# Kernel optimization log

Measured on AMD Instinct MI355X. Metric: run time of the kernel, lower is better.

## Reference

```python
import jax, jax.numpy as jnp
import numpy as np

D_MODEL = 128
REDUCTION = 4
KSIZE = 3
B = D_MODEL  # required by the original code's groups=B conv shape constraint
L = 4096


def setup_inputs() -> dict:
    key = jax.random.key(0)
    ks = jax.random.split(key, 7)
    d, r, K = D_MODEL, REDUCTION, KSIZE
    return {
        "x": jax.random.normal(ks[0], (B, L, d), dtype=jnp.float32),
        "W1": jax.random.normal(ks[1], (d // r, d), dtype=jnp.float32) * (1.0 / np.sqrt(d)),
        "b1": jax.random.normal(ks[2], (d // r,), dtype=jnp.float32) * 0.01,
        "W2": jax.random.normal(ks[3], (K, d // r), dtype=jnp.float32) * (1.0 / np.sqrt(d // r)),
        "b2": jax.random.normal(ks[4], (K,), dtype=jnp.float32) * 0.01,
        "Wc": jax.random.normal(ks[5], (d, d), dtype=jnp.float32) * (1.0 / np.sqrt(d)),
        "bc": jax.random.normal(ks[6], (d,), dtype=jnp.float32) * 0.01,
    }


def reference(x, W1, b1, W2, b2, Wc, bc):
    # x: [B, L, d] with B == d (required by original groups=B conv)
    Bsz, Lseq, d = x.shape
    K = W2.shape[0]
    pad = (K - 1) // 2
    # kernel generation from global average pool
    m = x.mean(axis=1)                                   # [B, d]
    h = jax.nn.gelu(m @ W1.T + b1, approximate=False)    # [B, d//r]
    w = jax.nn.softmax(h @ W2.T + b2, axis=-1)           # [B, K]; row j is the kernel for channel j
    # depthwise-style cross-correlation: y[b, l, c] = sum_k xp[b, l+k, c] * w[c, k]
    xp = jnp.pad(x, ((0, 0), (pad, pad), (0, 0)))        # [B, L+2*pad, d]
    y = sum(xp[:, k:k + Lseq, :] * w[None, None, :, k] for k in range(K))  # [B, L, d]
    # pointwise conv (kernel_size=1) == per-token linear
    return y @ Wc.T + bc                                 # [B, L, d]
```

## Files before the change

### kernel.cpp

```cpp
#include <hip/hip_runtime.h>
#include <hip/hip_bf16.h>

#define D_MODEL 128
#define SEQ_L   4096
#define BATCH   128
#define NSTRIP  2
#define STRIP   (SEQ_L / NSTRIP)
#define NBLK    (BATCH * NSTRIP)

typedef float f4 __attribute__((ext_vector_type(4)));
typedef float f32x4 __attribute__((ext_vector_type(4)));
typedef short bf16x8 __attribute__((ext_vector_type(8)));

__device__ __forceinline__ unsigned short f2bf(float f) {
    union { float f; unsigned u; } v; v.f = f;
    unsigned r = v.u + 0x7FFFu + ((v.u >> 16) & 1u);
    return (unsigned short)(r >> 16);
}

__device__ __forceinline__ void gridbar(int* ctr) {
    __syncthreads();
    if (threadIdx.x == 0) {
        __threadfence();
        atomicAdd(ctr, 1);
        while (__hip_atomic_load(ctr, __ATOMIC_ACQUIRE, __HIP_MEMORY_SCOPE_AGENT) < NBLK)
            __builtin_amdgcn_s_sleep(1);
    }
    __syncthreads();
    __threadfence();
}

template<bool GUARD>
__device__ __forceinline__ void load6(const float* __restrict__ xb, int gr0, int c4, f4 R[6]) {
    #pragma unroll
    for (int j = 0; j < 6; ++j) {
        int gr = gr0 + j;
        if (GUARD) {
            bool ok = (gr >= 0) && (gr < SEQ_L);
            int grc = ok ? gr : 0;
            f4 v = reinterpret_cast<const f4*>(xb + (size_t)grc * D_MODEL)[c4];
            f4 z = {0.f, 0.f, 0.f, 0.f};
            R[j] = ok ? v : z;
        } else {
            R[j] = reinterpret_cast<const f4*>(xb + (size_t)gr * D_MODEL)[c4];
        }
    }
}

__global__ __launch_bounds__(512, 2) void fused(const float* __restrict__ x,
                                                const float* __restrict__ W1,
                                                const float* __restrict__ b1,
                                                const float* __restrict__ W2,
                                                const float* __restrict__ b2,
                                                const float* __restrict__ Wc,
                                                const float* __restrict__ bc,
                                                float* __restrict__ out,
                                                int* __restrict__ ctr,
                                                float* __restrict__ part) {
    __shared__ f4 red[512];
    __shared__ __align__(16) unsigned short y_lds[2][64][132];
    __shared__ __align__(16) float wv_lds[3][128];

    const int t = threadIdx.x, gid = blockIdx.x;
    const int b = gid >> 1, strip = gid & 1;
    const int sb = strip * STRIP;
    const float* xb = x + (size_t)b * SEQ_L * D_MODEL;
    float* outb = out + (size_t)b * SEQ_L * D_MODEL;

    {
        int c4 = t & 31, ph = t >> 5;
        const f4* xv = reinterpret_cast<const f4*>(xb);
        f4 acc = {0.f, 0.f, 0.f, 0.f};
        for (int o = 0; o < STRIP / 128; ++o) {
            f4 R[8];
            #pragma unroll
            for (int j = 0; j < 8; ++j)
                R[j] = xv[(size_t)(sb + o * 128 + ph + j * 16) * 32 + c4];
            R[0] += R[4]; R[1] += R[5]; R[2] += R[6]; R[3] += R[7];
            R[0] += R[2]; R[1] += R[3];
            acc += R[0] + R[1];
        }
        red[t] = acc;
        __syncthreads();
        if (t < 32) {
            f4 s = red[t];
            #pragma unroll
            for (int p = 1; p < 16; ++p) s += red[t + 32 * p];
            reinterpret_cast<f4*>(part + ((size_t)b * NSTRIP + strip) * D_MODEL)[t] = s;
        }
    }
    gridbar(ctr);

    {
        int c = t >> 2, p = t & 3;
        f4 mv[8];
        #pragma unroll
        for (int d4 = 0; d4 < 8; ++d4) mv[d4] = (f4){0.f, 0.f, 0.f, 0.f};
        #pragma unroll
        for (int s = 0; s < NSTRIP; ++s) {
            const f4* ps = reinterpret_cast<const f4*>(part + ((size_t)c * NSTRIP + s) * D_MODEL + p * 32);
            #pragma unroll
            for (int d4 = 0; d4 < 8; ++d4) mv[d4] += ps[d4];
        }
        #pragma unroll
        for (int d4 = 0; d4 < 8; ++d4) mv[d4] *= (1.0f / (float)SEQ_L);

        float h[32];
        #pragma unroll
        for (int j = 0; j < 32; ++j) {
            const f4* w1r = reinterpret_cast<const f4*>(W1 + j * 128 + p * 32);
            f4 s4 = {0.f, 0.f, 0.f, 0.f};
            #pragma unroll
            for (int d4 = 0; d4 < 8; ++d4) s4 += mv[d4] * w1r[d4];
            float s = s4[0] + s4[1] + s4[2] + s4[3];
            s += __shfl_xor(s, 1);
            s += __shfl_xor(s, 2);
            s += b1[j];
            h[j] = 0.5f * s * (1.0f + erff(s * 0.70710678118654752f));
        }
        if (p == 0) {
            float lg[3], mx = -1e30f;
            #pragma unroll
            for (int k = 0; k < 3; ++k) {
                float s = b2[k];
                #pragma unroll
                for (int j = 0; j < 32; ++j) s += h[j] * W2[k * 32 + j];
                lg[k] = s; mx = fmaxf(mx, s);
            }
            float e[3], den = 0.f;
            #pragma unroll
            for (int k = 0; k < 3; ++k) { e[k] = __expf(lg[k] - mx); den += e[k]; }
            float inv = 1.0f / den;
            #pragma unroll
            for (int k = 0; k < 3; ++k) wv_lds[k][c] = e[k] * inv;
        }
    }
    __syncthreads();

    {
        int c4 = t & 31, rg = t >> 5;
        int lane = t & 63, wid = t >> 6;
        int r = lane & 15, q = lane >> 4, kb = q * 8;
        int co0 = wid * 16;

        f4 w0 = *reinterpret_cast<const f4*>(&wv_lds[0][c4 * 4]);
        f4 w1 = *reinterpret_cast<const f4*>(&wv_lds[1][c4 * 4]);
        f4 w2 = *reinterpret_cast<const f4*>(&wv_lds[2][c4 * 4]);

        bf16x8 awc[4];
        #pragma unroll
        for (int kc = 0; kc < 4; ++kc) {
            const float* wr = Wc + (size_t)(co0 + r) * D_MODEL + kc * 32 + kb;
            f4 a = *reinterpret_cast<const f4*>(wr);
            f4 bb = *reinterpret_cast<const f4*>(wr + 4);
            bf16x8 fr;
            fr[0] = (short)f2bf(a[0]); fr[1] = (short)f2bf(a[1]);
            fr[2] = (short)f2bf(a[2]); fr[3] = (short)f2bf(a[3]);
            fr[4] = (short)f2bf(bb[0]); fr[5] = (short)f2bf(bb[1]);
            fr[6] = (short)f2bf(bb[2]); fr[7] = (short)f2bf(bb[3]);
            awc[kc] = fr;
        }

        f4 bcv = *reinterpret_cast<const f4*>(bc + co0 + q * 4);

        f4 R[6];
        if (sb == 0) load6<true>(xb, sb + rg * 4 - 1, c4, R);
        else         load6<false>(xb, sb + rg * 4 - 1, c4, R);

        for (int ht = 0; ht < STRIP / 64; ++ht) {
            const int buf = ht & 1;
            int base = sb + ht * 64;
            #pragma unroll
            for (int j = 0; j < 4; ++j) {
                f4 y = R[j] * w0 + R[j + 1] * w1 + R[j + 2] * w2;
                ushort4 yb;
                yb.x = f2bf(y[0]); yb.y = f2bf(y[1]); yb.z = f2bf(y[2]); yb.w = f2bf(y[3]);
                *reinterpret_cast<ushort4*>(&y_lds[buf][rg * 4 + j][c4 * 4]) = yb;
            }
            if (ht < STRIP / 64 - 1) {
                int nb = base + 64;
                if (nb + 64 == SEQ_L) load6<true>(xb, nb + rg * 4 - 1, c4, R);
                else                  load6<false>(xb, nb + rg * 4 - 1, c4, R);
            }
            __syncthreads();

            f32x4 acc[4];
            #pragma unroll
            for (int g = 0; g < 4; ++g) acc[g] = (f32x4){0.f, 0.f, 0.f, 0.f};
            #pragma unroll
            for (int g = 0; g < 4; ++g)
                #pragma unroll
                for (int kc = 0; kc < 4; ++kc) {
                    bf16x8 bv = *reinterpret_cast<const bf16x8*>(&y_lds[buf][g * 16 + r][kc * 32 + kb]);
                    acc[g] = __builtin_amdgcn_mfma_f32_16x16x32_bf16(awc[kc], bv, acc[g], 0, 0, 0);
                }

            #pragma unroll
            for (int g = 0; g < 4; ++g) {
                int tok = base + g * 16 + r;
                *reinterpret_cast<f4*>(outb + (size_t)tok * D_MODEL + co0 + q * 4) = acc[g] + bcv;
            }
            __syncthreads();
        }
    }
}

extern "C" void kernel_launch(void* const* d_in, const int* in_sizes, int n_in,
                              void* d_out, int out_size, void* d_ws, size_t ws_size,
                              hipStream_t stream) {
    const float* x  = (const float*)d_in[0];
    const float* W1 = (const float*)d_in[1];
    const float* b1 = (const float*)d_in[2];
    const float* W2 = (const float*)d_in[3];
    const float* b2 = (const float*)d_in[4];
    const float* Wc = (const float*)d_in[5];
    const float* bc = (const float*)d_in[6];
    float* out = (float*)d_out;

    char* ws = (char*)d_ws;
    int* ctr = (int*)ws;
    float* part = (float*)(ws + 1024);

    hipMemsetAsync(ctr, 0, 128, stream);
    fused<<<NBLK, 512, 0, stream>>>(x, W1, b1, W2, b2, Wc, bc, out, ctr, part);
}
```

Measured before the change: 271.6 us.

## Split fused grid-barrier kernel into separate mean and conv kernels with finer grids

Replaces the single persistent kernel, which used a software grid barrier across 256 blocks, with two launches. The first computes per-segment channel sums over 8 segments per batch. The second tiles each sequence into 512-token blocks, recomputing the small MLP and softmax per block before the depthwise conv and the MFMA pointwise GEMM. This removes the grid-wide spin barrier and raises the block count to improve latency hiding and load balance. It also double-buffers the register prefetch and drops the second __syncthreads per tile. The cost is redundant MLP and Wc-conversion work in every conv block, plus an extra launch.

```diff
diff --git a/kernel.cpp b/kernel.cpp
--- a/kernel.cpp
+++ b/kernel.cpp
@@ -4,9 +4,8 @@
 #define D_MODEL 128
 #define SEQ_L   4096
 #define BATCH   128
-#define NSTRIP  2
-#define STRIP   (SEQ_L / NSTRIP)
-#define NBLK    (BATCH * NSTRIP)
+#define NSEG    8
+#define TOKS2   512
 
 typedef float f4 __attribute__((ext_vector_type(4)));
 typedef float f32x4 __attribute__((ext_vector_type(4)));
@@ -18,16 +17,33 @@
     return (unsigned short)(r >> 16);
 }
 
-__device__ __forceinline__ void gridbar(int* ctr) {
+__global__ __launch_bounds__(256) void kmean(const float* __restrict__ x,
+                                             float* __restrict__ part) {
+    int seg = blockIdx.x, b = blockIdx.y, t = threadIdx.x;
+    int c4 = t & 31, ph = t >> 5;
+    const f4* xb = reinterpret_cast<const f4*>(x + (size_t)b * SEQ_L * D_MODEL);
+    int l0 = seg * (SEQ_L / NSEG);
+
+    f4 acc = {0.f, 0.f, 0.f, 0.f};
+    #pragma unroll
+    for (int o = 0; o < (SEQ_L / NSEG) / 64; ++o) {
+        f4 R[8];
+        #pragma unroll
+        for (int j = 0; j < 8; ++j)
+            R[j] = xb[(size_t)(l0 + o * 64 + ph + j * 8) * 32 + c4];
+        R[0] += R[4]; R[1] += R[5]; R[2] += R[6]; R[3] += R[7];
+        R[0] += R[2]; R[1] += R[3];
+        acc += R[0] + R[1];
+    }
+    __shared__ f4 red[256];
+    red[t] = acc;
     __syncthreads();
-    if (threadIdx.x == 0) {
-        __threadfence();
-        atomicAdd(ctr, 1);
-        while (__hip_atomic_load(ctr, __ATOMIC_ACQUIRE, __HIP_MEMORY_SCOPE_AGENT) < NBLK)
-            __builtin_amdgcn_s_sleep(1);
-    }
-    __syncthreads();
-    __threadfence();
+    if (t < 32) {
+        f4 s = red[t];
+        #pragma unroll
+        for (int p = 1; p < 8; ++p) s += red[t + 32 * p];
+        reinterpret_cast<f4*>(part + ((size_t)b * NSEG + seg) * D_MODEL)[t] = s;
+    }
 }
 
 template<bool GUARD>
@@ -47,49 +63,31 @@
     }
 }
 
-__global__ __launch_bounds__(512, 2) void fused(const float* __restrict__ x,
+__global__ __launch_bounds__(512, 2) void kconv(const float* __restrict__ x,
+                                                const float* __restrict__ part,
                                                 const float* __restrict__ W1,
                                                 const float* __restrict__ b1,
                                                 const float* __restrict__ W2,
                                                 const float* __restrict__ b2,
                                                 const float* __restrict__ Wc,
                                                 const float* __restrict__ bc,
-                                                float* __restrict__ out,
-                                                int* __restrict__ ctr,
-                                                float* __restrict__ part) {
-    __shared__ f4 red[512];
+                                                float* __restrict__ out) {
     __shared__ __align__(16) unsigned short y_lds[2][64][132];
     __shared__ __align__(16) float wv_lds[3][128];
 
-    const int t = threadIdx.x, gid = blockIdx.x;
-    const int b = gid >> 1, strip = gid & 1;
-    const int sb = strip * STRIP;
+    const int t = threadIdx.x, b = blockIdx.y;
+    const int sb = blockIdx.x * TOKS2;
     const float* xb = x + (size_t)b * SEQ_L * D_MODEL;
     float* outb = out + (size_t)b * SEQ_L * D_MODEL;
 
-    {
-        int c4 = t & 31, ph = t >> 5;
-        const f4* xv = reinterpret_cast<const f4*>(xb);
-        f4 acc = {0.f, 0.f, 0.f, 0.f};
-        for (int o = 0; o < STRIP / 128; ++o) {
-            f4 R[8];
-            #pragma unroll
-            for (int j = 0; j < 8; ++j)
-                R[j] = xv[(size_t)(sb + o * 128 + ph + j * 16) * 32 + c4];
-            R[0] += R[4]; R[1] += R[5]; R[2] += R[6]; R[3] += R[7];
-            R[0] += R[2]; R[1] += R[3];
-            acc += R[0] + R[1];
-        }
-        red[t] = acc;
-        __syncthreads();
-        if (t < 32) {
-            f4 s = red[t];
-            #pragma unroll
-            for (int p = 1; p < 16; ++p) s += red[t + 32 * p];
-            reinterpret_cast<f4*>(part + ((size_t)b * NSTRIP + strip) * D_MODEL)[t] = s;
-        }
-    }
-    gridbar(ctr);
+    int c4 = t & 31, rg = t >> 5;
+    int lane = t & 63, wid = t >> 6;
+    int r = lane & 15, q = lane >> 4, kb = q * 8;
+    int co0 = wid * 16;
+
+    f4 R[2][6];
+    if (sb == 0) load6<true>(xb, sb + rg * 4 - 1, c4, R[0]);
+    else         load6<false>(xb, sb + rg * 4 - 1, c4, R[0]);
 
     {
         int c = t >> 2, p = t & 3;
@@ -97,8 +95,8 @@
         #pragma unroll
         for (int d4 = 0; d4 < 8; ++d4) mv[d4] = (f4){0.f, 0.f, 0.f, 0.f};
         #pragma unroll
-        for (int s = 0; s < NSTRIP; ++s) {
-            const f4* ps = reinterpret_cast<const f4*>(part + ((size_t)c * NSTRIP + s) * D_MODEL + p * 32);
+        for (int s = 0; s < NSEG; ++s) {
+            const f4* ps = reinterpret_cast<const f4*>(part + ((size_t)c * NSEG + s) * D_MODEL + p * 32);
             #pragma unroll
             for (int d4 = 0; d4 < 8; ++d4) mv[d4] += ps[d4];
         }
@@ -137,70 +135,58 @@
     }
     __syncthreads();
 
-    {
-        int c4 = t & 31, rg = t >> 5;
-        int lane = t & 63, wid = t >> 6;
-        int r = lane & 15, q = lane >> 4, kb = q * 8;
-        int co0 = wid * 16;
-
-        f4 w0 = *reinterpret_cast<const f4*>(&wv_lds[0][c4 * 4]);
-        f4 w1 = *reinterpret_cast<const f4*>(&wv_lds[1][c4 * 4]);
-        f4 w2 = *reinterpret_cast<const f4*>(&wv_lds[2][c4 * 4]);
-
-        bf16x8 awc[4];
-        #pragma unroll
-        for (int kc = 0; kc < 4; ++kc) {
-            const float* wr = Wc + (size_t)(co0 + r) * D_MODEL + kc * 32 + kb;
-            f4 a = *reinterpret_cast<const f4*>(wr);
-            f4 bb = *reinterpret_cast<const f4*>(wr + 4);
-            bf16x8 fr;
-            fr[0] = (short)f2bf(a[0]); fr[1] = (short)f2bf(a[1]);
-            fr[2] = (short)f2bf(a[2]); fr[3] = (short)f2bf(a[3]);
-            fr[4] = (short)f2bf(bb[0]); fr[5] = (short)f2bf(bb[1]);
-            fr[6] = (short)f2bf(bb[2]); fr[7] = (short)f2bf(bb[3]);
-            awc[kc] = fr;
-        }
-
-        f4 bcv = *reinterpret_cast<const f4*>(bc + co0 + q * 4);
-
-        f4 R[6];
-        if (sb == 0) load6<true>(xb, sb + rg * 4 - 1, c4, R);
-        else         load6<false>(xb, sb + rg * 4 - 1, c4, R);
-
-        for (int ht = 0; ht < STRIP / 64; ++ht) {
-            const int buf = ht & 1;
-            int base = sb + ht * 64;
-            #pragma unroll
-            for (int j = 0; j < 4; ++j) {
-                f4 y = R[j] * w0 + R[j + 1] * w1 + R[j + 2] * w2;
-                ushort4 yb;
-                yb.x = f2bf(y[0]); yb.y = f2bf(y[1]); yb.z = f2bf(y[2]); yb.w = f2bf(y[3]);
-                *reinterpret_cast<ushort4*>(&y_lds[buf][rg * 4 + j][c4 * 4]) = yb;
+    f4 w0 = *reinterpret_cast<const f4*>(&wv_lds[0][c4 * 4]);
+    f4 w1 = *reinterpret_cast<const f4*>(&wv_lds[1][c4 * 4]);
+    f4 w2 = *reinterpret_cast<const f4*>(&wv_lds[2][c4 * 4]);
+
+    bf16x8 awc[4];
+    #pragma unroll
+    for (int kc = 0; kc < 4; ++kc) {
+        const float* wr = Wc + (size_t)(co0 + r) * D_MODEL + kc * 32 + kb;
+        f4 a = *reinterpret_cast<const f4*>(wr);
+        f4 bb = *reinterpret_cast<const f4*>(wr + 4);
+        bf16x8 fr;
+        fr[0] = (short)f2bf(a[0]);  fr[1] = (short)f2bf(a[1]);
+        fr[2] = (short)f2bf(a[2]);  fr[3] = (short)f2bf(a[3]);
+        fr[4] = (short)f2bf(bb[0]); fr[5] = (short)f2bf(bb[1]);
+        fr[6] = (short)f2bf(bb[2]); fr[7] = (short)f2bf(bb[3]);
+        awc[kc] = fr;
+    }
+    f4 bcv = *reinterpret_cast<const f4*>(bc + co0 + q * 4);
+
+    #pragma unroll
+    for (int ht = 0; ht < TOKS2 / 64; ++ht) {
+        const int cur = ht & 1, nxt = cur ^ 1;
+        int base = sb + ht * 64;
+        if (ht < TOKS2 / 64 - 1) {
+            int nb = base + 64;
+            if (nb + 64 == SEQ_L) load6<true>(xb, nb + rg * 4 - 1, c4, R[nxt]);
+            else                  load6<false>(xb, nb + rg * 4 - 1, c4, R[nxt]);
+        }
+        #pragma unroll
+        for (int j = 0; j < 4; ++j) {
+            f4 y = R[cur][j] * w0 + R[cur][j + 1] * w1 + R[cur][j + 2] * w2;
+            ushort4 yb;
+            yb.x = f2bf(y[0]); yb.y = f2bf(y[1]); yb.z = f2bf(y[2]); yb.w = f2bf(y[3]);
+            *reinterpret_cast<ushort4*>(&y_lds[cur][rg * 4 + j][c4 * 4]) = yb;
+        }
+        __syncthreads();
+
+        f32x4 acc[4];
+        #pragma unroll
+        for (int g = 0; g < 4; ++g) acc[g] = (f32x4){0.f, 0.f, 0.f, 0.f};
+        #pragma unroll
+        for (int g = 0; g < 4; ++g)
+            #pragma unroll
+            for (int kc = 0; kc < 4; ++kc) {
+                bf16x8 bv = *reinterpret_cast<const bf16x8*>(&y_lds[cur][g * 16 + r][kc * 32 + kb]);
+                acc[g] = __builtin_amdgcn_mfma_f32_16x16x32_bf16(awc[kc], bv, acc[g], 0, 0, 0);
             }
-            if (ht < STRIP / 64 - 1) {
-                int nb = base + 64;
-                if (nb + 64 == SEQ_L) load6<true>(xb, nb + rg * 4 - 1, c4, R);
-                else                  load6<false>(xb, nb + rg * 4 - 1, c4, R);
-            }
-            __syncthreads();
-
-            f32x4 acc[4];
-            #pragma unroll
-            for (int g = 0; g < 4; ++g) acc[g] = (f32x4){0.f, 0.f, 0.f, 0.f};
-            #pragma unroll
-            for (int g = 0; g < 4; ++g)
-                #pragma unroll
-                for (int kc = 0; kc < 4; ++kc) {
-                    bf16x8 bv = *reinterpret_cast<const bf16x8*>(&y_lds[buf][g * 16 + r][kc * 32 + kb]);
-                    acc[g] = __builtin_amdgcn_mfma_f32_16x16x32_bf16(awc[kc], bv, acc[g], 0, 0, 0);
-                }
-
-            #pragma unroll
-            for (int g = 0; g < 4; ++g) {
-                int tok = base + g * 16 + r;
-                *reinterpret_cast<f4*>(outb + (size_t)tok * D_MODEL + co0 + q * 4) = acc[g] + bcv;
-            }
-            __syncthreads();
+
+        #pragma unroll
+        for (int g = 0; g < 4; ++g) {
+            int tok = base + g * 16 + r;
+            *reinterpret_cast<f4*>(outb + (size_t)tok * D_MODEL + co0 + q * 4) = acc[g] + bcv;
         }
     }
 }
@@ -217,10 +203,8 @@
     const float* bc = (const float*)d_in[6];
     float* out = (float*)d_out;
 
-    char* ws = (char*)d_ws;
-    int* ctr = (int*)ws;
-    float* part = (float*)(ws + 1024);
-
-    hipMemsetAsync(ctr, 0, 128, stream);
-    fused<<<NBLK, 512, 0, stream>>>(x, W1, b1, W2, b2, Wc, bc, out, ctr, part);
-}
+    float* part = (float*)d_ws;
+
+    kmean<<<dim3(NSEG, BATCH), 256, 0, stream>>>(x, part);
+    kconv<<<dim3(SEQ_L / TOKS2, BATCH), 512, 0, stream>>>(x, part, W1, b1, W2, b2, Wc, bc, out);
+}
```

Result: slower. 447.5 us (+64.8%).
